# Kernel optimization log

Measured on AMD Instinct MI355X. Metric: run time of the kernel, lower is better.

## Reference

```python
import jax, jax.numpy as jnp
import numpy as np


def _conv3x3(x, w, b):
    # NCHW conv, stride 1, padding 1 == SAME for 3x3
    y = jax.lax.conv_general_dilated(
        x, w, window_strides=(1, 1), padding='SAME',
        dimension_numbers=('NCHW', 'OIHW', 'NCHW'))
    return y + b[None, :, None, None]


def setup_inputs() -> dict:
    key = jax.random.key(0)
    k_x, k_w1, k_b1, k_w2, k_b2 = jax.random.split(key, 5)
    B, T, C, H, W = 4, 16, 128, 112, 112  # C = 2 * in_channels
    x = jax.random.normal(k_x, (B, T, C, H, W), dtype=jnp.float32)
    # PredictorLG_conv(embed_dim=2*in_channels): Conv2d(128,2,3) -> GELU -> Conv2d(2,2,3) -> GELU -> Softmax(dim=1)
    w1 = jax.random.normal(k_w1, (2, C, 3, 3), dtype=jnp.float32) * 0.05
    b1 = jax.random.normal(k_b1, (2,), dtype=jnp.float32) * 0.05
    w2 = jax.random.normal(k_w2, (2, 2, 3, 3), dtype=jnp.float32) * 0.05
    b2 = jax.random.normal(k_b2, (2,), dtype=jnp.float32) * 0.05
    return {"x": x, "w1": w1, "b1": b1, "w2": w2, "b2": b2}


def reference(x, w1, b1, w2, b2):
    # spatch branch of PatchNet_ms_conv.forward
    B, T, C, H, W = x.shape
    xf = x.reshape(B * T, C, H, W)  # (b t c h w) -> ((b t) c h w)
    s = jax.nn.gelu(_conv3x3(xf, w1, b1), approximate=False)
    s = jax.nn.gelu(_conv3x3(s, w2, b2), approximate=False)
    s = jax.nn.softmax(s, axis=1)  # nn.Softmax() on 4D -> dim=1
    x1, x2 = jnp.split(xf, 2, axis=1)  # chunk(2, dim=-3)
    xa = s[:, 0:1] * x1 + s[:, 1:2] * x2  # ((b t), c//2, h, w)
    # '(b t) c h w -> b c t h w'
    xa = xa.reshape(B, T, C // 2, H, W).transpose(0, 2, 1, 3, 4)
    return xa
```

## Files before the change

kernel.cpp:

```cpp
#include <hip/hip_runtime.h>
#include <math.h>
#include <stdint.h>

#define HW    112
#define HW2   (112 * 112)
#define NIMG  64
#define CIN   128
#define NKG   2
#define ICG   (CIN / NKG)
#define TILEP 2032
#define NSLOT 4
#define NWG   (2 * ICG * 9)

__device__ __forceinline__ float gelu_exact(float v) {
    return 0.5f * v * (1.0f + erff(v * 0.70710678118654752f));
}

__global__ __launch_bounds__(256) void k1_partial(
    const float* __restrict__ x, const float* __restrict__ w1,
    float* __restrict__ part) {
    __shared__ __align__(16) float tile[NSLOT][TILEP];
    __shared__ float wlds[NWG];

    const int tid = threadIdx.x;
    const int bx  = blockIdx.x;
    const int n   = blockIdx.y;
    const int kg  = blockIdx.z;
    const int h0  = bx * 16;
    const int icb = kg * ICG;

    const int tx   = tid & 15;
    const int ty   = tid >> 4;
    const int col0 = tx * 7;

    for (int j = tid; j < NWG; j += 256) {
        const int oc   = j / (ICG * 9);
        const int rest = j - oc * (ICG * 9);
        wlds[j] = w1[(size_t)oc * CIN * 9 + (size_t)icb * 9 + rest];
    }
    if (bx == 0 && tid < HW) {
#pragma unroll
        for (int s = 0; s < NSLOT; ++s) tile[s][tid] = 0.f;
    }
    if (bx == 6 && tid < HW) {
#pragma unroll
        for (int s = 0; s < NSLOT; ++s) tile[s][17 * HW + tid] = 0.f;
    }

    const int    ldsoff = (bx == 0) ? HW : 0;
    const int    count4 = (bx == 0 || bx == 6) ? 476 : 504;
    const size_t srcoff = (bx == 0) ? 0 : (size_t)(h0 - 1) * HW;
    const float* xn = x + ((size_t)n * CIN + icb) * HW2 + srcoff;

    const float lmask = (col0 > 0) ? 1.f : 0.f;
    const float rmask = (col0 + 7 < HW) ? 1.f : 0.f;
    const int   loff  = (col0 > 0) ? -1 : 0;
    const int   roff  = (col0 + 7 < HW) ? 7 : 0;

    float acc0[7] = {0.f, 0.f, 0.f, 0.f, 0.f, 0.f, 0.f};
    float acc1[7] = {0.f, 0.f, 0.f, 0.f, 0.f, 0.f, 0.f};

#define STAGE(CH, SLOT)                                                        \
    do {                                                                       \
        const float* _src = xn + (size_t)(CH) * HW2;                           \
        float* _dst = &tile[(SLOT)][ldsoff];                                   \
        _Pragma("unroll")                                                      \
        for (int _r = 0; _r < 2; ++_r) {                                       \
            const int _i = tid + _r * 256;                                     \
            if (_i < count4)                                                   \
                __builtin_amdgcn_global_load_lds(                              \
                    (const __attribute__((address_space(1))) unsigned int*)(_src + (size_t)_i * 4), \
                    (__attribute__((address_space(3))) unsigned int*)(_dst + _i * 4), \
                    16, 0, 0);                                                 \
        }                                                                      \
    } while (0)

    STAGE(0, 0);
    STAGE(1, 1);
    STAGE(2, 2);
    STAGE(3, 3);
    asm volatile("s_waitcnt lgkmcnt(0)" ::: "memory");

    int slot = 0;
#pragma unroll 1
    for (int ic = 0; ic < ICG; ++ic) {
        if (ic < ICG - 3)       asm volatile("s_waitcnt vmcnt(6)" ::: "memory");
        else if (ic == ICG - 3) asm volatile("s_waitcnt vmcnt(4)" ::: "memory");
        else if (ic == ICG - 2) asm volatile("s_waitcnt vmcnt(2)" ::: "memory");
        else                    asm volatile("s_waitcnt vmcnt(0)" ::: "memory");
        __builtin_amdgcn_s_barrier();
        __builtin_amdgcn_sched_barrier(0);

        const float* tl  = tile[slot];
        const float* wap = wlds + ic * 9;
        const float* wbp = wlds + ICG * 9 + ic * 9;
#pragma unroll
        for (int dr = 0; dr < 3; ++dr) {
            const int base = (ty + dr) * HW + col0;
            float v[9];
            v[0] = tl[base + loff] * lmask;
#pragma unroll
            for (int k = 1; k <= 7; ++k) v[k] = tl[base + (k - 1)];
            v[8] = tl[base + roff] * rmask;
            const float a0 = wap[dr * 3 + 0], a1 = wap[dr * 3 + 1], a2 = wap[dr * 3 + 2];
            const float c0 = wbp[dr * 3 + 0], c1 = wbp[dr * 3 + 1], c2 = wbp[dr * 3 + 2];
#pragma unroll
            for (int j = 0; j < 7; ++j) {
                acc0[j] += a0 * v[j] + a1 * v[j + 1] + a2 * v[j + 2];
                acc1[j] += c0 * v[j] + c1 * v[j + 1] + c2 * v[j + 2];
            }
        }

        asm volatile("s_waitcnt lgkmcnt(0)" ::: "memory");
        __builtin_amdgcn_sched_barrier(0);
        __builtin_amdgcn_s_barrier();
        if (ic + NSLOT < ICG) STAGE(ic + NSLOT, slot);
        slot = (slot + 1) & (NSLOT - 1);
    }
#undef STAGE

    const size_t obase = ((size_t)kg * NIMG + n) * 2;
    float* p0 = part + (obase + 0) * HW2 + (size_t)(h0 + ty) * HW + col0;
    float* p1 = part + (obase + 1) * HW2 + (size_t)(h0 + ty) * HW + col0;
#pragma unroll
    for (int j = 0; j < 7; ++j) { p0[j] = acc0[j]; p1[j] = acc1[j]; }
}

__global__ __launch_bounds__(256) void k1b_reduce_gelu(
    const float* __restrict__ part, const float* __restrict__ b1,
    float* __restrict__ g, int total4) {
    int idx = blockIdx.x * blockDim.x + threadIdx.x;
    if (idx >= total4) return;
    const size_t stride = (size_t)NIMG * 2 * HW2;
    const size_t e = (size_t)idx * 4;
    const int oc = (int)((e / HW2) & 1);
    float4 s = *reinterpret_cast<const float4*>(part + e);
#pragma unroll
    for (int kg = 1; kg < NKG; ++kg) {
        const float4 p = *reinterpret_cast<const float4*>(part + kg * stride + e);
        s.x += p.x; s.y += p.y; s.z += p.z; s.w += p.w;
    }
    const float bb = b1[oc];
    float4 o;
    o.x = gelu_exact(s.x + bb);
    o.y = gelu_exact(s.y + bb);
    o.z = gelu_exact(s.z + bb);
    o.w = gelu_exact(s.w + bb);
    *reinterpret_cast<float4*>(g + e) = o;
}

__global__ __launch_bounds__(448) void k1_conv1_gelu(
    const float* __restrict__ x, const float* __restrict__ w1,
    const float* __restrict__ b1, float* __restrict__ g) {
    const int n  = blockIdx.y;
    const int h  = blockIdx.x * 16 + threadIdx.y;
    const int w0 = threadIdx.x * 4;
    float acc0[4], acc1[4];
    const float bb0 = b1[0], bb1 = b1[1];
#pragma unroll
    for (int j = 0; j < 4; ++j) { acc0[j] = bb0; acc1[j] = bb1; }
    const float* xn = x + (size_t)n * CIN * HW2;
#pragma unroll 4
    for (int ic = 0; ic < CIN; ++ic) {
        const float* xc = xn + (size_t)ic * HW2;
        const float* wa = w1 + ic * 9;
        const float* wb = w1 + (CIN + ic) * 9;
#pragma unroll
        for (int dh = -1; dh <= 1; ++dh) {
            const int hh = h + dh;
            if (hh < 0 || hh >= HW) continue;
            const float* xr = xc + hh * HW;
            const float4 c4  = *reinterpret_cast<const float4*>(xr + w0);
            const float left  = (w0 > 0)      ? xr[w0 - 1] : 0.0f;
            const float right = (w0 + 4 < HW) ? xr[w0 + 4] : 0.0f;
            const float v0 = left, v1 = c4.x, v2 = c4.y, v3 = c4.z, v4 = c4.w, v5 = right;
            const int r = (dh + 1) * 3;
            const float a0 = wa[r], a1 = wa[r + 1], a2 = wa[r + 2];
            const float c0 = wb[r], c1 = wb[r + 1], c2 = wb[r + 2];
            acc0[0] += a0 * v0 + a1 * v1 + a2 * v2;
            acc0[1] += a0 * v1 + a1 * v2 + a2 * v3;
            acc0[2] += a0 * v2 + a1 * v3 + a2 * v4;
            acc0[3] += a0 * v3 + a1 * v4 + a2 * v5;
            acc1[0] += c0 * v0 + c1 * v1 + c2 * v2;
            acc1[1] += c0 * v1 + c1 * v2 + c2 * v3;
            acc1[2] += c0 * v2 + c1 * v3 + c2 * v4;
            acc1[3] += c0 * v3 + c1 * v4 + c2 * v5;
        }
    }
    float4 o0, o1;
    o0.x = gelu_exact(acc0[0]); o0.y = gelu_exact(acc0[1]);
    o0.z = gelu_exact(acc0[2]); o0.w = gelu_exact(acc0[3]);
    o1.x = gelu_exact(acc1[0]); o1.y = gelu_exact(acc1[1]);
    o1.z = gelu_exact(acc1[2]); o1.w = gelu_exact(acc1[3]);
    float* g0 = g + (size_t)(n * 2 + 0) * HW2 + h * HW + w0;
    float* g1 = g + (size_t)(n * 2 + 1) * HW2 + h * HW + w0;
    *reinterpret_cast<float4*>(g0) = o0;
    *reinterpret_cast<float4*>(g1) = o1;
}

__global__ __launch_bounds__(448) void k23_conv2_blend(
    const float* __restrict__ g, const float* __restrict__ w2,
    const float* __restrict__ b2, const float* __restrict__ x,
    float* __restrict__ out) {
    __shared__ __align__(16) float gs[2][18 * HW];

    const int tid = threadIdx.x;
    const int bx  = blockIdx.x;
    const int n   = blockIdx.y;
    const int h0  = bx * 16;

    for (int i = tid; i < 1008; i += 448) {
        const int ch  = i / 504;
        const int rem = i - ch * 504;
        const int r   = rem / 28;
        const int c4  = rem - r * 28;
        const int hh  = h0 - 1 + r;
        float4 v = make_float4(0.f, 0.f, 0.f, 0.f);
        if (hh >= 0 && hh < HW)
            v = *reinterpret_cast<const float4*>(
                g + ((size_t)(n * 2 + ch) * HW + hh) * HW + c4 * 4);
        *reinterpret_cast<float4*>(&gs[ch][r * HW + c4 * 4]) = v;
    }
    __syncthreads();

    const int row  = tid / 28;
    const int col0 = (tid - row * 28) * 4;
    const float lm = (col0 > 0) ? 1.f : 0.f;
    const float rm = (col0 + 4 < HW) ? 1.f : 0.f;
    const int   lo = (col0 > 0) ? -1 : 0;
    const int   ro = (col0 + 4 < HW) ? 1 : 0;

    float accA[4], accB[4];
    const float bb0 = b2[0], bb1 = b2[1];
#pragma unroll
    for (int j = 0; j < 4; ++j) { accA[j] = bb0; accB[j] = bb1; }

#pragma unroll
    for (int ch = 0; ch < 2; ++ch) {
        const float* wa = w2 + ch * 9;
        const float* wb = w2 + (2 + ch) * 9;
#pragma unroll
        for (int dr = 0; dr < 3; ++dr) {
            const int base = (row + dr) * HW + col0;
            const float4 c4 = *reinterpret_cast<const float4*>(&gs[ch][base]);
            const float v0 = gs[ch][base + lo] * lm;
            const float v5 = gs[ch][base + 3 + ro] * rm;
            const float v1 = c4.x, v2 = c4.y, v3 = c4.z, v4 = c4.w;
            const float a0 = wa[dr * 3], a1 = wa[dr * 3 + 1], a2 = wa[dr * 3 + 2];
            const float c0 = wb[dr * 3], c1 = wb[dr * 3 + 1], c2 = wb[dr * 3 + 2];
            accA[0] += a0 * v0 + a1 * v1 + a2 * v2;
            accA[1] += a0 * v1 + a1 * v2 + a2 * v3;
            accA[2] += a0 * v2 + a1 * v3 + a2 * v4;
            accA[3] += a0 * v3 + a1 * v4 + a2 * v5;
            accB[0] += c0 * v0 + c1 * v1 + c2 * v2;
            accB[1] += c0 * v1 + c1 * v2 + c2 * v3;
            accB[2] += c0 * v2 + c1 * v3 + c2 * v4;
            accB[3] += c0 * v3 + c1 * v4 + c2 * v5;
        }
    }

    float4 s;
    s.x = 1.0f / (1.0f + expf(gelu_exact(accB[0]) - gelu_exact(accA[0])));
    s.y = 1.0f / (1.0f + expf(gelu_exact(accB[1]) - gelu_exact(accA[1])));
    s.z = 1.0f / (1.0f + expf(gelu_exact(accB[2]) - gelu_exact(accA[2])));
    s.w = 1.0f / (1.0f + expf(gelu_exact(accB[3]) - gelu_exact(accA[3])));

    const int b = n >> 4, t = n & 15;
    const size_t px = (size_t)(h0 + row) * HW + col0;
    const float* x1p = x + ((size_t)n * CIN) * HW2 + px;
    const float* x2p = x1p + (size_t)64 * HW2;
    float* op = out + (((size_t)(b * 64) * 16 + t) * HW2) + px;
#pragma unroll 4
    for (int c = 0; c < 64; ++c) {
        const float4 x1 = *reinterpret_cast<const float4*>(x1p);
        const float4 x2 = *reinterpret_cast<const float4*>(x2p);
        float4 o;
        o.x = s.x * x1.x + (1.0f - s.x) * x2.x;
        o.y = s.y * x1.y + (1.0f - s.y) * x2.y;
        o.z = s.z * x1.z + (1.0f - s.z) * x2.z;
        o.w = s.w * x1.w + (1.0f - s.w) * x2.w;
        *reinterpret_cast<float4*>(op) = o;
        x1p += HW2; x2p += HW2; op += (size_t)16 * HW2;
    }
}

extern "C" void kernel_launch(void* const* d_in, const int* in_sizes, int n_in,
                              void* d_out, int out_size, void* d_ws, size_t ws_size,
                              hipStream_t stream) {
    const float* x  = (const float*)d_in[0];
    const float* w1 = (const float*)d_in[1];
    const float* b1 = (const float*)d_in[2];
    const float* w2 = (const float*)d_in[3];
    const float* b2 = (const float*)d_in[4];
    float* out = (float*)d_out;

    const size_t partF = (size_t)NKG * NIMG * 2 * HW2;
    const size_t gF    = (size_t)NIMG * 2 * HW2;
    const size_t need  = (partF + gF) * sizeof(float);

    dim3 grd(7, NIMG);

    float* g;
    if (ws_size >= need) {
        float* part = (float*)d_ws;
        g = part + partF;
        dim3 grdp(7, NIMG, NKG);
        k1_partial<<<grdp, 256, 0, stream>>>(x, w1, part);
        const int total4g = (int)(gF / 4);
        k1b_reduce_gelu<<<(total4g + 255) / 256, 256, 0, stream>>>(part, b1, g, total4g);
    } else {
        g = (float*)d_ws;
        dim3 blk(28, 16);
        k1_conv1_gelu<<<grd, blk, 0, stream>>>(x, w1, b1, g);
    }

    k23_conv2_blend<<<grd, 448, 0, stream>>>(g, w2, b2, x, out);
}
```

Measured before the change: 241.4 us.

## Split conv1 over 8 channel groups, fuse reduce into conv2, separate blend

Raises the number of input-channel groups for the first convolution from 2 to 8 and cuts the LDS ring to 3 slots. This gives more workgroups and higher occupancy on the x-streaming conv. The partial-sum reduction and GELU are folded into the conv2/softmax kernel, which writes a single mixing weight map. The blend moves into its own flat elementwise kernel with output-ordered indexing, so writes are contiguous. The risk is extra traffic for the larger partial buffer, plus one more launch.

```diff
diff --git a/kernel.cpp b/kernel.cpp
--- a/kernel.cpp
+++ b/kernel.cpp
@@ -6,10 +6,10 @@
 #define HW2   (112 * 112)
 #define NIMG  64
 #define CIN   128
-#define NKG   2
+#define NKG   8
 #define ICG   (CIN / NKG)
 #define TILEP 2032
-#define NSLOT 4
+#define NSLOT 3
 #define NWG   (2 * ICG * 9)
 
 __device__ __forceinline__ float gelu_exact(float v) {
@@ -78,14 +78,12 @@
     STAGE(0, 0);
     STAGE(1, 1);
     STAGE(2, 2);
-    STAGE(3, 3);
     asm volatile("s_waitcnt lgkmcnt(0)" ::: "memory");
 
     int slot = 0;
 #pragma unroll 1
     for (int ic = 0; ic < ICG; ++ic) {
-        if (ic < ICG - 3)       asm volatile("s_waitcnt vmcnt(6)" ::: "memory");
-        else if (ic == ICG - 3) asm volatile("s_waitcnt vmcnt(4)" ::: "memory");
+        if (ic < ICG - 2)       asm volatile("s_waitcnt vmcnt(4)" ::: "memory");
         else if (ic == ICG - 2) asm volatile("s_waitcnt vmcnt(2)" ::: "memory");
         else                    asm volatile("s_waitcnt vmcnt(0)" ::: "memory");
         __builtin_amdgcn_s_barrier();
@@ -115,7 +113,7 @@
         __builtin_amdgcn_sched_barrier(0);
         __builtin_amdgcn_s_barrier();
         if (ic + NSLOT < ICG) STAGE(ic + NSLOT, slot);
-        slot = (slot + 1) & (NSLOT - 1);
+        slot = (slot == NSLOT - 1) ? 0 : slot + 1;
     }
 #undef STAGE
 
@@ -126,27 +124,85 @@
     for (int j = 0; j < 7; ++j) { p0[j] = acc0[j]; p1[j] = acc1[j]; }
 }
 
-__global__ __launch_bounds__(256) void k1b_reduce_gelu(
+__global__ __launch_bounds__(448) void k2f_reduce_conv2(
     const float* __restrict__ part, const float* __restrict__ b1,
-    float* __restrict__ g, int total4) {
-    int idx = blockIdx.x * blockDim.x + threadIdx.x;
-    if (idx >= total4) return;
-    const size_t stride = (size_t)NIMG * 2 * HW2;
-    const size_t e = (size_t)idx * 4;
-    const int oc = (int)((e / HW2) & 1);
-    float4 s = *reinterpret_cast<const float4*>(part + e);
-#pragma unroll
-    for (int kg = 1; kg < NKG; ++kg) {
-        const float4 p = *reinterpret_cast<const float4*>(part + kg * stride + e);
-        s.x += p.x; s.y += p.y; s.z += p.z; s.w += p.w;
-    }
-    const float bb = b1[oc];
+    const float* __restrict__ w2, const float* __restrict__ b2,
+    float* __restrict__ s0) {
+    __shared__ __align__(16) float gs[2][18 * HW];
+
+    const int tid = threadIdx.x;
+    const int bx  = blockIdx.x;
+    const int n   = blockIdx.y;
+    const int h0  = bx * 16;
+    const size_t kstride = (size_t)NIMG * 2 * HW2;
+
+    for (int i = tid; i < 1008; i += 448) {
+        const int ch  = i / 504;
+        const int rem = i - ch * 504;
+        const int r   = rem / 28;
+        const int c4  = rem - r * 28;
+        const int hh  = h0 - 1 + r;
+        float4 v = make_float4(0.f, 0.f, 0.f, 0.f);
+        if (hh >= 0 && hh < HW) {
+            const float* p = part + ((size_t)n * 2 + ch) * HW2 + (size_t)hh * HW + c4 * 4;
+            float4 a = *reinterpret_cast<const float4*>(p);
+#pragma unroll
+            for (int kg = 1; kg < NKG; ++kg) {
+                const float4 q = *reinterpret_cast<const float4*>(p + kg * kstride);
+                a.x += q.x; a.y += q.y; a.z += q.z; a.w += q.w;
+            }
+            const float bb = b1[ch];
+            v.x = gelu_exact(a.x + bb);
+            v.y = gelu_exact(a.y + bb);
+            v.z = gelu_exact(a.z + bb);
+            v.w = gelu_exact(a.w + bb);
+        }
+        *reinterpret_cast<float4*>(&gs[ch][r * HW + c4 * 4]) = v;
+    }
+    __syncthreads();
+
+    const int row  = tid / 28;
+    const int col0 = (tid - row * 28) * 4;
+    const float lm = (col0 > 0) ? 1.f : 0.f;
+    const float rm = (col0 + 4 < HW) ? 1.f : 0.f;
+    const int   lo = (col0 > 0) ? -1 : 0;
+    const int   ro = (col0 + 4 < HW) ? 1 : 0;
+
+    float accA[4], accB[4];
+    const float bb0 = b2[0], bb1 = b2[1];
+#pragma unroll
+    for (int j = 0; j < 4; ++j) { accA[j] = bb0; accB[j] = bb1; }
+
+#pragma unroll
+    for (int ch = 0; ch < 2; ++ch) {
+        const float* wa = w2 + ch * 9;
+        const float* wb = w2 + (2 + ch) * 9;
+#pragma unroll
+        for (int dr = 0; dr < 3; ++dr) {
+            const int base = (row + dr) * HW + col0;
+            const float4 c4 = *reinterpret_cast<const float4*>(&gs[ch][base]);
+            const float v0 = gs[ch][base + lo] * lm;
+            const float v5 = gs[ch][base + 3 + ro] * rm;
+            const float v1 = c4.x, v2 = c4.y, v3 = c4.z, v4 = c4.w;
+            const float a0 = wa[dr * 3], a1 = wa[dr * 3 + 1], a2 = wa[dr * 3 + 2];
+            const float c0 = wb[dr * 3], c1 = wb[dr * 3 + 1], c2 = wb[dr * 3 + 2];
+            accA[0] += a0 * v0 + a1 * v1 + a2 * v2;
+            accA[1] += a0 * v1 + a1 * v2 + a2 * v3;
+            accA[2] += a0 * v2 + a1 * v3 + a2 * v4;
+            accA[3] += a0 * v3 + a1 * v4 + a2 * v5;
+            accB[0] += c0 * v0 + c1 * v1 + c2 * v2;
+            accB[1] += c0 * v1 + c1 * v2 + c2 * v3;
+            accB[2] += c0 * v2 + c1 * v3 + c2 * v4;
+            accB[3] += c0 * v3 + c1 * v4 + c2 * v5;
+        }
+    }
+
     float4 o;
-    o.x = gelu_exact(s.x + bb);
-    o.y = gelu_exact(s.y + bb);
-    o.z = gelu_exact(s.z + bb);
-    o.w = gelu_exact(s.w + bb);
-    *reinterpret_cast<float4*>(g + e) = o;
+    o.x = 1.0f / (1.0f + expf(gelu_exact(accB[0]) - gelu_exact(accA[0])));
+    o.y = 1.0f / (1.0f + expf(gelu_exact(accB[1]) - gelu_exact(accA[1])));
+    o.z = 1.0f / (1.0f + expf(gelu_exact(accB[2]) - gelu_exact(accA[2])));
+    o.w = 1.0f / (1.0f + expf(gelu_exact(accB[3]) - gelu_exact(accA[3])));
+    *reinterpret_cast<float4*>(s0 + (size_t)n * HW2 + (size_t)(h0 + row) * HW + col0) = o;
 }
 
 __global__ __launch_bounds__(448) void k1_conv1_gelu(
@@ -198,56 +254,33 @@
     *reinterpret_cast<float4*>(g1) = o1;
 }
 
-__global__ __launch_bounds__(448) void k23_conv2_blend(
+__global__ __launch_bounds__(448) void k2_conv2_softmax(
     const float* __restrict__ g, const float* __restrict__ w2,
-    const float* __restrict__ b2, const float* __restrict__ x,
-    float* __restrict__ out) {
-    __shared__ __align__(16) float gs[2][18 * HW];
-
-    const int tid = threadIdx.x;
-    const int bx  = blockIdx.x;
-    const int n   = blockIdx.y;
-    const int h0  = bx * 16;
-
-    for (int i = tid; i < 1008; i += 448) {
-        const int ch  = i / 504;
-        const int rem = i - ch * 504;
-        const int r   = rem / 28;
-        const int c4  = rem - r * 28;
-        const int hh  = h0 - 1 + r;
-        float4 v = make_float4(0.f, 0.f, 0.f, 0.f);
-        if (hh >= 0 && hh < HW)
-            v = *reinterpret_cast<const float4*>(
-                g + ((size_t)(n * 2 + ch) * HW + hh) * HW + c4 * 4);
-        *reinterpret_cast<float4*>(&gs[ch][r * HW + c4 * 4]) = v;
-    }
-    __syncthreads();
-
-    const int row  = tid / 28;
-    const int col0 = (tid - row * 28) * 4;
-    const float lm = (col0 > 0) ? 1.f : 0.f;
-    const float rm = (col0 + 4 < HW) ? 1.f : 0.f;
-    const int   lo = (col0 > 0) ? -1 : 0;
-    const int   ro = (col0 + 4 < HW) ? 1 : 0;
-
+    const float* __restrict__ b2, float* __restrict__ s0) {
+    const int n  = blockIdx.y;
+    const int h  = blockIdx.x * 16 + threadIdx.y;
+    const int w0 = threadIdx.x * 4;
     float accA[4], accB[4];
     const float bb0 = b2[0], bb1 = b2[1];
 #pragma unroll
     for (int j = 0; j < 4; ++j) { accA[j] = bb0; accB[j] = bb1; }
-
-#pragma unroll
-    for (int ch = 0; ch < 2; ++ch) {
-        const float* wa = w2 + ch * 9;
-        const float* wb = w2 + (2 + ch) * 9;
-#pragma unroll
-        for (int dr = 0; dr < 3; ++dr) {
-            const int base = (row + dr) * HW + col0;
-            const float4 c4 = *reinterpret_cast<const float4*>(&gs[ch][base]);
-            const float v0 = gs[ch][base + lo] * lm;
-            const float v5 = gs[ch][base + 3 + ro] * rm;
-            const float v1 = c4.x, v2 = c4.y, v3 = c4.z, v4 = c4.w;
-            const float a0 = wa[dr * 3], a1 = wa[dr * 3 + 1], a2 = wa[dr * 3 + 2];
-            const float c0 = wb[dr * 3], c1 = wb[dr * 3 + 1], c2 = wb[dr * 3 + 2];
+#pragma unroll
+    for (int c = 0; c < 2; ++c) {
+        const float* gc = g + (size_t)(n * 2 + c) * HW2;
+        const float* wa = w2 + c * 9;
+        const float* wb = w2 + (2 + c) * 9;
+#pragma unroll
+        for (int dh = -1; dh <= 1; ++dh) {
+            const int hh = h + dh;
+            if (hh < 0 || hh >= HW) continue;
+            const float* gr = gc + hh * HW;
+            const float4 c4  = *reinterpret_cast<const float4*>(gr + w0);
+            const float left  = (w0 > 0)      ? gr[w0 - 1] : 0.0f;
+            const float right = (w0 + 4 < HW) ? gr[w0 + 4] : 0.0f;
+            const float v0 = left, v1 = c4.x, v2 = c4.y, v3 = c4.z, v4 = c4.w, v5 = right;
+            const int r = (dh + 1) * 3;
+            const float a0 = wa[r], a1 = wa[r + 1], a2 = wa[r + 2];
+            const float c0 = wb[r], c1 = wb[r + 1], c2 = wb[r + 2];
             accA[0] += a0 * v0 + a1 * v1 + a2 * v2;
             accA[1] += a0 * v1 + a1 * v2 + a2 * v3;
             accA[2] += a0 * v2 + a1 * v3 + a2 * v4;
@@ -258,30 +291,39 @@
             accB[3] += c0 * v3 + c1 * v4 + c2 * v5;
         }
     }
-
-    float4 s;
-    s.x = 1.0f / (1.0f + expf(gelu_exact(accB[0]) - gelu_exact(accA[0])));
-    s.y = 1.0f / (1.0f + expf(gelu_exact(accB[1]) - gelu_exact(accA[1])));
-    s.z = 1.0f / (1.0f + expf(gelu_exact(accB[2]) - gelu_exact(accA[2])));
-    s.w = 1.0f / (1.0f + expf(gelu_exact(accB[3]) - gelu_exact(accA[3])));
-
-    const int b = n >> 4, t = n & 15;
-    const size_t px = (size_t)(h0 + row) * HW + col0;
-    const float* x1p = x + ((size_t)n * CIN) * HW2 + px;
-    const float* x2p = x1p + (size_t)64 * HW2;
-    float* op = out + (((size_t)(b * 64) * 16 + t) * HW2) + px;
-#pragma unroll 4
-    for (int c = 0; c < 64; ++c) {
-        const float4 x1 = *reinterpret_cast<const float4*>(x1p);
-        const float4 x2 = *reinterpret_cast<const float4*>(x2p);
-        float4 o;
-        o.x = s.x * x1.x + (1.0f - s.x) * x2.x;
-        o.y = s.y * x1.y + (1.0f - s.y) * x2.y;
-        o.z = s.z * x1.z + (1.0f - s.z) * x2.z;
-        o.w = s.w * x1.w + (1.0f - s.w) * x2.w;
-        *reinterpret_cast<float4*>(op) = o;
-        x1p += HW2; x2p += HW2; op += (size_t)16 * HW2;
-    }
+    float4 o;
+    o.x = 1.0f / (1.0f + expf(gelu_exact(accB[0]) - gelu_exact(accA[0])));
+    o.y = 1.0f / (1.0f + expf(gelu_exact(accB[1]) - gelu_exact(accA[1])));
+    o.z = 1.0f / (1.0f + expf(gelu_exact(accB[2]) - gelu_exact(accA[2])));
+    o.w = 1.0f / (1.0f + expf(gelu_exact(accB[3]) - gelu_exact(accA[3])));
+    *reinterpret_cast<float4*>(s0 + (size_t)n * HW2 + h * HW + w0) = o;
+}
+
+__global__ __launch_bounds__(256) void k3_blend(
+    const float* __restrict__ x, const float* __restrict__ s0,
+    float* __restrict__ out, int total4) {
+    int idx = blockIdx.x * blockDim.x + threadIdx.x;
+    if (idx >= total4) return;
+    const int W4 = HW / 4;
+    int w4  = idx % W4;
+    int tmp = idx / W4;
+    int h   = tmp % HW; tmp /= HW;
+    int t   = tmp % 16; tmp /= 16;
+    int c   = tmp % 64;
+    int b   = tmp / 64;
+    const int n = b * 16 + t;
+
+    const size_t px = (size_t)h * HW + w4 * 4;
+    const float4 x1 = *reinterpret_cast<const float4*>(x + (size_t)(n * CIN + c)      * HW2 + px);
+    const float4 x2 = *reinterpret_cast<const float4*>(x + (size_t)(n * CIN + c + 64) * HW2 + px);
+    const float4 s  = *reinterpret_cast<const float4*>(s0 + (size_t)n * HW2 + px);
+
+    float4 o;
+    o.x = s.x * x1.x + (1.0f - s.x) * x2.x;
+    o.y = s.y * x1.y + (1.0f - s.y) * x2.y;
+    o.z = s.z * x1.z + (1.0f - s.z) * x2.z;
+    o.w = s.w * x1.w + (1.0f - s.w) * x2.w;
+    *reinterpret_cast<float4*>(out + (size_t)idx * 4) = o;
 }
 
 extern "C" void kernel_launch(void* const* d_in, const int* in_sizes, int n_in,
@@ -296,23 +338,26 @@
 
     const size_t partF = (size_t)NKG * NIMG * 2 * HW2;
     const size_t gF    = (size_t)NIMG * 2 * HW2;
-    const size_t need  = (partF + gF) * sizeof(float);
+    const size_t s0F   = (size_t)NIMG * HW2;
+    const size_t need  = (partF + s0F) * sizeof(float);
 
     dim3 grd(7, NIMG);
-
-    float* g;
+    float* s0;
+
     if (ws_size >= need) {
         float* part = (float*)d_ws;
-        g = part + partF;
+        s0 = part + partF;
         dim3 grdp(7, NIMG, NKG);
         k1_partial<<<grdp, 256, 0, stream>>>(x, w1, part);
-        const int total4g = (int)(gF / 4);
-        k1b_reduce_gelu<<<(total4g + 255) / 256, 256, 0, stream>>>(part, b1, g, total4g);
+        k2f_reduce_conv2<<<grd, 448, 0, stream>>>(part, b1, w2, b2, s0);
     } else {
-        g = (float*)d_ws;
+        float* g = (float*)d_ws;
+        s0 = g + gF;
         dim3 blk(28, 16);
         k1_conv1_gelu<<<grd, blk, 0, stream>>>(x, w1, b1, g);
-    }
-
-    k23_conv2_blend<<<grd, 448, 0, stream>>>(g, w2, b2, x, out);
-}
+        k2_conv2_softmax<<<grd, blk, 0, stream>>>(g, w2, b2, s0);
+    }
+
+    const int total4 = 4 * 64 * 16 * HW * (HW / 4);
+    k3_blend<<<(total4 + 255) / 256, 256, 0, stream>>>(x, s0, out, total4);
+}
```

New measurement: 217.9 us. 1.11x faster.
